# Kernel tuning notes

Measured on AMD Instinct MI355X. Metric: run time of the kernel, lower is better.

Reference implementation:

```python
import jax, jax.numpy as jnp
import numpy as np
from jax import lax

DN = ('NCHW', 'OIHW', 'NCHW')


def _dwconv(x, w, pad_h, pad_w):
    # depthwise conv: feature_group_count == channels
    C = x.shape[1]
    return lax.conv_general_dilated(
        x, w, window_strides=(1, 1),
        padding=[(pad_h, pad_h), (pad_w, pad_w)],
        dimension_numbers=DN, feature_group_count=C)


def setup_inputs() -> dict:
    key = jax.random.key(0)
    ks = jax.random.split(key, 6)
    B, C, H, W = 8, 64, 256, 256
    K = 21
    x = jax.random.normal(ks[0], (B, C, H, W), dtype=jnp.float32)
    local_w = jax.random.normal(ks[1], (C, 1, 5, 5), dtype=jnp.float32) * (2.0 / 25) ** 0.5
    h_w = jax.random.normal(ks[2], (C, 1, 1, K), dtype=jnp.float32) * (2.0 / K) ** 0.5
    v_w = jax.random.normal(ks[3], (C, 1, K, 1), dtype=jnp.float32) * (2.0 / K) ** 0.5
    pw_w = jax.random.normal(ks[4], (C, C, 1, 1), dtype=jnp.float32) * (1.0 / C) ** 0.5
    gamma = jnp.ones((C,), dtype=jnp.float32)
    beta = jnp.zeros((C,), dtype=jnp.float32)
    mean = jnp.zeros((C,), dtype=jnp.float32)
    var = jnp.ones((C,), dtype=jnp.float32)
    return {"x": x, "local_w": local_w, "h_w": h_w, "v_w": v_w,
            "pw_w": pw_w, "gamma": gamma, "beta": beta, "mean": mean, "var": var}


def reference(x, local_w, h_w, v_w, pw_w, gamma, beta, mean, var):
    eps = 1e-5
    attn = _dwconv(x, local_w, 2, 2)        # 5x5 depthwise
    attn = _dwconv(attn, h_w, 0, 10)        # 1x21 depthwise
    attn = _dwconv(attn, v_w, 10, 0)        # 21x1 depthwise
    attn = lax.conv_general_dilated(        # 1x1 pointwise (full mix)
        attn, pw_w, (1, 1), [(0, 0), (0, 0)], dimension_numbers=DN)
    # BatchNorm (inference mode with running stats) fused with sigmoid gate
    inv = gamma * lax.rsqrt(var + eps)
    attn = attn * inv[None, :, None, None] + (beta - mean * inv)[None, :, None, None]
    return x * jax.nn.sigmoid(attn)
```

## Files before the change

### kernel.cpp

```cpp
#include <hip/hip_runtime.h>
#include <hip/hip_bf16.h>

#define BB 8
#define CC 64
#define HH 256
#define WW 256

__device__ __forceinline__ unsigned short f2bf(float f) {
    __hip_bfloat16 h = __float2bfloat16(f);
    return *reinterpret_cast<unsigned short*>(&h);
}
__device__ __forceinline__ float bf2f(unsigned short u) {
    unsigned int v = ((unsigned int)u) << 16;
    float r;
    __builtin_memcpy(&r, &v, 4);
    return r;
}

__global__ __launch_bounds__(512) void k1_local_h(
        const float* __restrict__ x, const float* __restrict__ lw,
        const float* __restrict__ hw, unsigned short* __restrict__ a2out) {
    const int strip = blockIdx.x;
    const int bc    = blockIdx.y;
    const int c     = bc & (CC - 1);
    const int y0    = strip * 8;
    const int tid   = threadIdx.x;

    __shared__ float xs[12][264];
    __shared__ float a1[8][276];

    const float* xbase = x + (size_t)bc * HH * WW;
    for (int i = tid; i < 12 * 260; i += 512) {
        int rr = i / 260, ccx = i - rr * 260;
        int gy = y0 - 2 + rr, gx = ccx - 2;
        float v = 0.f;
        if (gy >= 0 && gy < HH && gx >= 0 && gx < WW) v = xbase[gy * WW + gx];
        xs[rr][ccx] = v;
    }
    for (int i = tid; i < 8 * 20; i += 512) {
        int rr = i / 20, jj = i - rr * 20;
        a1[rr][jj < 10 ? jj : (256 + jj)] = 0.f;
    }
    __syncthreads();

    const int r = tid >> 6;
    const int l = tid & 63;
    const float* lwc = lw + c * 25;

    float acc[4] = {0.f, 0.f, 0.f, 0.f};
    #pragma unroll
    for (int ky = 0; ky < 5; ++ky) {
        float row[8];
        #pragma unroll
        for (int j = 0; j < 8; ++j) row[j] = xs[r + ky][4 * l + j];
        #pragma unroll
        for (int kx = 0; kx < 5; ++kx) {
            float wv = lwc[ky * 5 + kx];
            #pragma unroll
            for (int j = 0; j < 4; ++j) acc[j] = fmaf(wv, row[j + kx], acc[j]);
        }
    }
    #pragma unroll
    for (int j = 0; j < 4; ++j) a1[r][10 + 4 * l + j] = acc[j];
    __syncthreads();

    float wnd[24];
    #pragma unroll
    for (int i = 0; i < 24; ++i) wnd[i] = a1[r][4 * l + i];
    float o[4] = {0.f, 0.f, 0.f, 0.f};
    const float* hwc = hw + c * 21;
    #pragma unroll
    for (int k = 0; k < 21; ++k) {
        float wv = hwc[k];
        #pragma unroll
        for (int j = 0; j < 4; ++j) o[j] = fmaf(wv, wnd[j + k], o[j]);
    }

    unsigned short* dst = a2out + (size_t)(bc * HH + y0 + r) * WW + 4 * l;
    ushort4 pk;
    pk.x = f2bf(o[0]); pk.y = f2bf(o[1]); pk.z = f2bf(o[2]); pk.w = f2bf(o[3]);
    *reinterpret_cast<ushort4*>(dst) = pk;
}

__global__ __launch_bounds__(256) void k2a_v(
        const unsigned short* __restrict__ a2, const float* __restrict__ vw,
        unsigned short* __restrict__ a3) {
    const int strip = blockIdx.x;
    const int bc    = blockIdx.y;
    const int c     = bc & (CC - 1);
    const int y0    = strip * 32;
    const int xcol  = threadIdx.x;
    const float* vwc = vw + c * 21;

    float acc[32];
    #pragma unroll
    for (int i = 0; i < 32; ++i) acc[i] = 0.f;

    const unsigned short* src = a2 + (size_t)bc * HH * WW + xcol;
    #pragma unroll
    for (int rr = 0; rr < 52; ++rr) {
        int gy = y0 + rr - 10;
        float v = 0.f;
        if (gy >= 0 && gy < HH) v = bf2f(src[gy * WW]);
        #pragma unroll
        for (int k = 0; k < 21; ++k) {
            int yl = rr - k;
            if (yl >= 0 && yl < 32) acc[yl] = fmaf(vwc[k], v, acc[yl]);
        }
    }
    unsigned short* dst = a3 + (size_t)bc * HH * WW + (size_t)y0 * WW + xcol;
    #pragma unroll
    for (int y = 0; y < 32; ++y) dst[y * WW] = f2bf(acc[y]);
}

__global__ __launch_bounds__(256) void k2b_pw(
        const unsigned short* __restrict__ a3, const float* __restrict__ x,
        const float* __restrict__ pw, const float* __restrict__ gamma,
        const float* __restrict__ beta, const float* __restrict__ mean,
        const float* __restrict__ var, float* __restrict__ out) {
    const int y   = blockIdx.x;
    const int b   = blockIdx.y;
    const int tid = threadIdx.x;

    __shared__ unsigned short a3s[64][256];

    const unsigned short* abase = a3 + ((size_t)b * CC * HH + y) * WW;
    for (int i = tid; i < 64 * 64; i += 256) {
        int ci = i >> 6, q = (i & 63) << 2;
        ushort4 v = *reinterpret_cast<const ushort4*>(abase + (size_t)ci * HH * WW + q);
        *reinterpret_cast<ushort4*>(&a3s[ci][q]) = v;
    }
    __syncthreads();

    const int wu = __builtin_amdgcn_readfirstlane(tid >> 6);
    const int l  = tid & 63;

    float acc[64];
    #pragma unroll
    for (int i = 0; i < 64; ++i) acc[i] = 0.f;

    #pragma unroll 4
    for (int ci = 0; ci < 64; ++ci) {
        ushort4 raw = *reinterpret_cast<const ushort4*>(&a3s[ci][l << 2]);
        float p0 = bf2f(raw.x), p1 = bf2f(raw.y), p2 = bf2f(raw.z), p3 = bf2f(raw.w);
        #pragma unroll
        for (int j = 0; j < 16; ++j) {
            float wv = pw[(wu * 16 + j) * 64 + ci];
            acc[j * 4 + 0] = fmaf(wv, p0, acc[j * 4 + 0]);
            acc[j * 4 + 1] = fmaf(wv, p1, acc[j * 4 + 1]);
            acc[j * 4 + 2] = fmaf(wv, p2, acc[j * 4 + 2]);
            acc[j * 4 + 3] = fmaf(wv, p3, acc[j * 4 + 3]);
        }
    }

    #pragma unroll
    for (int j = 0; j < 16; ++j) {
        int co = wu * 16 + j;
        float inv = gamma[co] * rsqrtf(var[co] + 1e-5f);
        float sh  = beta[co] - mean[co] * inv;
        size_t off = (((size_t)b * CC + co) * HH + y) * WW + (l << 2);
        float4 xv = *reinterpret_cast<const float4*>(x + off);
        float4 r;
        float a;
        a = acc[j * 4 + 0] * inv + sh; r.x = xv.x / (1.f + __expf(-a));
        a = acc[j * 4 + 1] * inv + sh; r.y = xv.y / (1.f + __expf(-a));
        a = acc[j * 4 + 2] * inv + sh; r.z = xv.z / (1.f + __expf(-a));
        a = acc[j * 4 + 3] * inv + sh; r.w = xv.w / (1.f + __expf(-a));
        *reinterpret_cast<float4*>(out + off) = r;
    }
}

extern "C" void kernel_launch(void* const* d_in, const int* in_sizes, int n_in,
                              void* d_out, int out_size, void* d_ws, size_t ws_size,
                              hipStream_t stream) {
    const float* x     = (const float*)d_in[0];
    const float* lw    = (const float*)d_in[1];
    const float* hw    = (const float*)d_in[2];
    const float* vw    = (const float*)d_in[3];
    const float* pw    = (const float*)d_in[4];
    const float* gamma = (const float*)d_in[5];
    const float* beta  = (const float*)d_in[6];
    const float* mean  = (const float*)d_in[7];
    const float* var   = (const float*)d_in[8];
    float* out = (float*)d_out;

    unsigned short* ws1 = (unsigned short*)d_ws;
    unsigned short* ws2 = ws1 + (size_t)BB * CC * HH * WW;

    k1_local_h<<<dim3(HH / 8, BB * CC), 512, 0, stream>>>(x, lw, hw, ws1);
    k2a_v<<<dim3(HH / 32, BB * CC), 256, 0, stream>>>(ws1, vw, ws2);
    k2b_pw<<<dim3(HH, BB), 256, 0, stream>>>(ws2, x, pw, gamma, beta, mean, var, out);
}
```

Before: 445.5 us.

## Use wave shuffles for horizontal conv halo and two columns per thread in vertical pass

The first kernel now loads the input tile row by row and reads the shared tile as float4 vectors. Its second shared buffer and the second barrier are gone: the 1x21 horizontal filter gets neighbour values across lanes with __shfl instead of staging them in LDS. The vertical kernel has each thread handle two adjacent columns using ushort2 loads and stores, with the block size halved, so memory accesses are wider. The cost is more registers (64 accumulators in the vertical kernel, the nb array in the first) and half as many threads per block in the vertical pass.

Measured after the change: 578.0 us. 29.7% more time.

```diff
diff --git a/kernel.cpp b/kernel.cpp
--- a/kernel.cpp
+++ b/kernel.cpp
@@ -25,55 +25,77 @@
     const int c     = bc & (CC - 1);
     const int y0    = strip * 8;
     const int tid   = threadIdx.x;
+    const int r     = tid >> 6;
+    const int l     = tid & 63;
 
     __shared__ float xs[12][264];
-    __shared__ float a1[8][276];
 
     const float* xbase = x + (size_t)bc * HH * WW;
-    for (int i = tid; i < 12 * 260; i += 512) {
-        int rr = i / 260, ccx = i - rr * 260;
-        int gy = y0 - 2 + rr, gx = ccx - 2;
-        float v = 0.f;
-        if (gy >= 0 && gy < HH && gx >= 0 && gx < WW) v = xbase[gy * WW + gx];
-        xs[rr][ccx] = v;
-    }
-    for (int i = tid; i < 8 * 20; i += 512) {
-        int rr = i / 20, jj = i - rr * 20;
-        a1[rr][jj < 10 ? jj : (256 + jj)] = 0.f;
+    for (int row = r; row < 12; row += 8) {
+        int gy = y0 - 2 + row;
+        bool rowok = (unsigned)gy < HH;
+        const float* xr = xbase + (rowok ? gy : 0) * WW;
+        #pragma unroll
+        for (int j = 0; j < 4; ++j) {
+            int i = l + 64 * j;
+            int gx = i - 2;
+            float v = (rowok && gx >= 0) ? xr[gx] : 0.f;
+            xs[row][i] = v;
+        }
+        if (l < 4) {
+            int i = 256 + l;
+            int gx = i - 2;
+            float v = (rowok && gx < WW) ? xr[gx] : 0.f;
+            xs[row][i] = v;
+        }
     }
     __syncthreads();
 
-    const int r = tid >> 6;
-    const int l = tid & 63;
     const float* lwc = lw + c * 25;
 
-    float acc[4] = {0.f, 0.f, 0.f, 0.f};
+    float p[4] = {0.f, 0.f, 0.f, 0.f};
     #pragma unroll
     for (int ky = 0; ky < 5; ++ky) {
-        float row[8];
-        #pragma unroll
-        for (int j = 0; j < 8; ++j) row[j] = xs[r + ky][4 * l + j];
+        const float4* rp = reinterpret_cast<const float4*>(&xs[r + ky][4 * l]);
+        float4 lo = rp[0], hi = rp[1];
+        float row[8] = {lo.x, lo.y, lo.z, lo.w, hi.x, hi.y, hi.z, hi.w};
         #pragma unroll
         for (int kx = 0; kx < 5; ++kx) {
             float wv = lwc[ky * 5 + kx];
             #pragma unroll
-            for (int j = 0; j < 4; ++j) acc[j] = fmaf(wv, row[j + kx], acc[j]);
-        }
-    }
-    #pragma unroll
-    for (int j = 0; j < 4; ++j) a1[r][10 + 4 * l + j] = acc[j];
-    __syncthreads();
-
-    float wnd[24];
-    #pragma unroll
-    for (int i = 0; i < 24; ++i) wnd[i] = a1[r][4 * l + i];
+            for (int j = 0; j < 4; ++j) p[j] = fmaf(wv, row[j + kx], p[j]);
+        }
+    }
+
+    float nb[7][4];
+    #pragma unroll
+    for (int d = -3; d <= 3; ++d) {
+        if (d == 0) {
+            #pragma unroll
+            for (int j = 0; j < 4; ++j) nb[3][j] = p[j];
+        } else {
+            int sl = l + d;
+            bool ok = (unsigned)sl < 64u;
+            #pragma unroll
+            for (int j = 0; j < 4; ++j) {
+                float v = __shfl(p[j], ok ? sl : 0);
+                nb[d + 3][j] = ok ? v : 0.f;
+            }
+        }
+    }
+
     float o[4] = {0.f, 0.f, 0.f, 0.f};
     const float* hwc = hw + c * 21;
     #pragma unroll
     for (int k = 0; k < 21; ++k) {
         float wv = hwc[k];
         #pragma unroll
-        for (int j = 0; j < 4; ++j) o[j] = fmaf(wv, wnd[j + k], o[j]);
+        for (int j = 0; j < 4; ++j) {
+            int m  = j + k - 10 + 12;
+            int d  = m >> 2;
+            int jj = m & 3;
+            o[j] = fmaf(wv, nb[d][jj], o[j]);
+        }
     }
 
     unsigned short* dst = a2out + (size_t)(bc * HH + y0 + r) * WW + 4 * l;
@@ -82,35 +104,46 @@
     *reinterpret_cast<ushort4*>(dst) = pk;
 }
 
-__global__ __launch_bounds__(256) void k2a_v(
+__global__ __launch_bounds__(128) void k2a_v(
         const unsigned short* __restrict__ a2, const float* __restrict__ vw,
         unsigned short* __restrict__ a3) {
     const int strip = blockIdx.x;
     const int bc    = blockIdx.y;
     const int c     = bc & (CC - 1);
     const int y0    = strip * 32;
-    const int xcol  = threadIdx.x;
+    const int t     = threadIdx.x;
     const float* vwc = vw + c * 21;
 
-    float acc[32];
-    #pragma unroll
-    for (int i = 0; i < 32; ++i) acc[i] = 0.f;
-
-    const unsigned short* src = a2 + (size_t)bc * HH * WW + xcol;
+    float accA[32], accB[32];
+    #pragma unroll
+    for (int i = 0; i < 32; ++i) { accA[i] = 0.f; accB[i] = 0.f; }
+
+    const ushort2* src = reinterpret_cast<const ushort2*>(a2 + (size_t)bc * HH * WW) + t;
     #pragma unroll
     for (int rr = 0; rr < 52; ++rr) {
         int gy = y0 + rr - 10;
-        float v = 0.f;
-        if (gy >= 0 && gy < HH) v = bf2f(src[gy * WW]);
+        float va = 0.f, vb = 0.f;
+        if ((unsigned)gy < HH) {
+            ushort2 v = src[gy * (WW / 2)];
+            va = bf2f(v.x); vb = bf2f(v.y);
+        }
         #pragma unroll
         for (int k = 0; k < 21; ++k) {
             int yl = rr - k;
-            if (yl >= 0 && yl < 32) acc[yl] = fmaf(vwc[k], v, acc[yl]);
-        }
-    }
-    unsigned short* dst = a3 + (size_t)bc * HH * WW + (size_t)y0 * WW + xcol;
-    #pragma unroll
-    for (int y = 0; y < 32; ++y) dst[y * WW] = f2bf(acc[y]);
+            if (yl >= 0 && yl < 32) {
+                float wv = vwc[k];
+                accA[yl] = fmaf(wv, va, accA[yl]);
+                accB[yl] = fmaf(wv, vb, accB[yl]);
+            }
+        }
+    }
+    ushort2* dst = reinterpret_cast<ushort2*>(a3 + (size_t)bc * HH * WW + (size_t)y0 * WW) + t;
+    #pragma unroll
+    for (int y = 0; y < 32; ++y) {
+        ushort2 o;
+        o.x = f2bf(accA[y]); o.y = f2bf(accB[y]);
+        dst[y * (WW / 2)] = o;
+    }
 }
 
 __global__ __launch_bounds__(256) void k2b_pw(
@@ -188,6 +221,6 @@
     unsigned short* ws2 = ws1 + (size_t)BB * CC * HH * WW;
 
     k1_local_h<<<dim3(HH / 8, BB * CC), 512, 0, stream>>>(x, lw, hw, ws1);
-    k2a_v<<<dim3(HH / 32, BB * CC), 256, 0, stream>>>(ws1, vw, ws2);
+    k2a_v<<<dim3(HH / 32, BB * CC), 128, 0, stream>>>(ws1, vw, ws2);
     k2b_pw<<<dim3(HH, BB), 256, 0, stream>>>(ws2, x, pw, gamma, beta, mean, var, out);
 }
```
